# Optimization experiments

Measured on AMD Instinct MI355X. Metric: run time of the kernel, lower is better.

The kernel has to match this reference:

```python
import jax, jax.numpy as jnp
import numpy as np

N = 50000      # nodes
E = 800000     # edges (avg degree 16)
D = 128        # in_dim
H = 128        # hidden_dim
C = 10         # num_classes
G = 128        # graphs in batch
NUM_LAYERS = 3


def setup_inputs() -> dict:
    key = jax.random.key(0)
    ks = jax.random.split(key, 32)
    inp = {
        'features': jax.random.normal(ks[0], (N, D), dtype=jnp.float32),
        'src': jax.random.randint(ks[1], (E,), 0, N, dtype=jnp.int32),
        'dst': jax.random.randint(ks[2], (E,), 0, N, dtype=jnp.int32),
        'graph_ids': jnp.sort(jax.random.randint(ks[3], (N,), 0, G, dtype=jnp.int32)),
        'eps': jnp.zeros((NUM_LAYERS,), dtype=jnp.float32),  # learn_eps=True, init 0
    }
    # GIN MLPs: layer i has linear1 [in,H], linear2 [H,H] (stored as [in,out])
    ki = 4
    for i in range(NUM_LAYERS):
        din = D if i == 0 else H
        inp[f'w1_{i}'] = jax.random.normal(ks[ki], (din, H), dtype=jnp.float32) * (1.0 / np.sqrt(din)); ki += 1
        inp[f'b1_{i}'] = jnp.zeros((H,), dtype=jnp.float32)
        inp[f'w2_{i}'] = jax.random.normal(ks[ki], (H, H), dtype=jnp.float32) * (1.0 / np.sqrt(H)); ki += 1
        inp[f'b2_{i}'] = jnp.zeros((H,), dtype=jnp.float32)
    inp['wc1'] = jax.random.normal(ks[ki], (H, H), dtype=jnp.float32) * (1.0 / np.sqrt(H)); ki += 1
    inp['bc1'] = jnp.zeros((H,), dtype=jnp.float32)
    inp['wc2'] = jax.random.normal(ks[ki], (H, C), dtype=jnp.float32) * (1.0 / np.sqrt(H)); ki += 1
    inp['bc2'] = jnp.zeros((C,), dtype=jnp.float32)
    return inp


def _mlp(x, w1, b1, w2, b2):
    return jax.nn.relu(x @ w1 + b1) @ w2 + b2


def reference(features, src, dst, graph_ids, eps,
              w1_0, b1_0, w2_0, b2_0,
              w1_1, b1_1, w2_1, b2_1,
              w1_2, b1_2, w2_2, b2_2,
              wc1, bc1, wc2, bc2):
    mlps = [(w1_0, b1_0, w2_0, b2_0), (w1_1, b1_1, w2_1, b2_1), (w1_2, b1_2, w2_2, b2_2)]
    h = features
    for i, (w1, b1, w2, b2) in enumerate(mlps):
        # GINConv: aggregate sum of in-neighbor features (gather src, segment-sum into dst)
        agg = jax.ops.segment_sum(h[src], dst, num_segments=N)
        h = (1.0 + eps[i]) * h + agg
        h = _mlp(h, w1, b1, w2, b2)
        h = jax.nn.relu(h)
    # SumPooling: nodes -> graphs
    hg = jax.ops.segment_sum(h, graph_ids, num_segments=G)  # [G, H]
    out = jax.nn.relu(hg @ wc1 + bc1) @ wc2 + bc2            # [G, C]
    return out
```

## Files before the change

### kernel.cpp

```cpp
#include <hip/hip_runtime.h>

#define NN 50000
#define EE 800000
#define HH 128
#define CC 10
#define GG 128
#define NBK 782
#define NCH 98
#define CHUNK 8192

typedef __attribute__((ext_vector_type(8))) short short8;
typedef __attribute__((ext_vector_type(4))) float f32x4;

__device__ __forceinline__ ushort f2b(float f) {
    union { float f; uint u; } x; x.f = f;
    uint u = x.u;
    uint r = (u + 0x7fffu + ((u >> 16) & 1u)) >> 16;
    return (ushort)r;
}
__device__ __forceinline__ float lo2f(uint v) {
    union { uint u; float f; } x; x.u = v << 16; return x.f;
}
__device__ __forceinline__ float hi2f(uint v) {
    union { uint u; float f; } x; x.u = v & 0xffff0000u; return x.f;
}


__global__ __launch_bounds__(256) void prep_kernel(const float* __restrict__ features,
                                                   const float* w0, const float* w1,
                                                   const float* w2, const float* w3,
                                                   const float* w4, const float* w5,
                                                   const int* __restrict__ dst,
                                                   ushort* __restrict__ hb0,
                                                   ushort* __restrict__ wt,
                                                   int* __restrict__ hist,
                                                   float* __restrict__ hg) {
    __shared__ int hc[NBK];
    const int b = blockIdx.x, t = threadIdx.x;
    if (b < 6250) {
        int idx = b * 256 + t;
        float4 v = *(const float4*)(features + (size_t)idx * 4);
        ushort4 o;
        o.x = f2b(v.x); o.y = f2b(v.y); o.z = f2b(v.z); o.w = f2b(v.w);
        *(ushort4*)(hb0 + (size_t)idx * 4) = o;
    } else if (b < 6634) {
        int idx = (b - 6250) * 256 + t;
        int mi = idx >> 14, rest = idx & 16383;
        int n = rest >> 7, k = rest & 127;
        const float* src;
        switch (mi) {
            case 0: src = w0; break; case 1: src = w1; break;
            case 2: src = w2; break; case 3: src = w3; break;
            case 4: src = w4; break; default: src = w5; break;
        }
        wt[mi * 16384 + n * 128 + k] = f2b(src[k * 128 + n]);
    } else if (b < 6732) {
        const int c = b - 6634;
        for (int k = t; k < NBK; k += 256) hc[k] = 0;
        __syncthreads();
        for (int j = 0; j < 32; ++j) {
            int e = c * CHUNK + j * 256 + t;
            if (e < EE) atomicAdd(&hc[dst[e] >> 6], 1);
        }
        __syncthreads();
        for (int k = t; k < NBK; k += 256) hist[k * NCH + c] = hc[k];
    } else {
        int idx = (b - 6732) * 256 + t;
        hg[idx] = 0.f;
    }
}

__global__ __launch_bounds__(128) void bscan_kernel(const int* __restrict__ hist,
                                                    int* __restrict__ rel,
                                                    int* __restrict__ btot) {
    __shared__ int s[128];
    const int b = blockIdx.x, t = threadIdx.x;
    int v = (t < NCH) ? hist[b * NCH + t] : 0;
    s[t] = v;
    __syncthreads();
    for (int off = 1; off < 128; off <<= 1) {
        int tt = (t >= off) ? s[t - off] : 0;
        __syncthreads();
        s[t] += tt;
        __syncthreads();
    }
    if (t < NCH) rel[b * NCH + t] = s[t] - v;
    if (t == 127) btot[b] = s[127];
}

__global__ __launch_bounds__(1024) void tscan_kernel(const int* __restrict__ btot,
                                                     int* __restrict__ bucketptr,
                                                     int* __restrict__ rowptr) {
    __shared__ int s[1024];
    const int t = threadIdx.x;
    int v = (t < NBK) ? btot[t] : 0;
    s[t] = v;
    __syncthreads();
    for (int off = 1; off < 1024; off <<= 1) {
        int tt = (t >= off) ? s[t - off] : 0;
        __syncthreads();
        s[t] += tt;
        __syncthreads();
    }
    if (t < NBK) bucketptr[t] = s[t] - v;
    if (t == 0) { bucketptr[NBK] = EE; rowptr[NN] = EE; }
}

__global__ __launch_bounds__(256) void scatter_kernel(const int* __restrict__ src,
                                                      const int* __restrict__ dst,
                                                      const int* __restrict__ rel,
                                                      const int* __restrict__ bucketptr,
                                                      int* __restrict__ epk) {
    __shared__ int cur[NBK];
    const int c = blockIdx.x, t = threadIdx.x;
    for (int k = t; k < NBK; k += 256) cur[k] = bucketptr[k] + rel[k * NCH + c];
    __syncthreads();
    for (int j = 0; j < 32; ++j) {
        int e = c * CHUNK + j * 256 + t;
        if (e < EE) {
            int d = dst[e];
            int bk = d >> 6;
            int pos = atomicAdd(&cur[bk], 1);
            epk[pos] = ((d & 63) << 16) | src[e];
        }
    }
}

__global__ __launch_bounds__(256) void bsort_kernel(const int* __restrict__ epk,
                                                    const int* __restrict__ bucketptr,
                                                    ushort* __restrict__ eidx,
                                                    int* __restrict__ rowptr) {
    __shared__ int cnt[64];
    __shared__ int cur[64];
    const int b = blockIdx.x, t = threadIdx.x;
    const int base = bucketptr[b], end = bucketptr[b + 1];
    if (t < 64) cnt[t] = 0;
    __syncthreads();
    for (int i = base + t; i < end; i += 256)
        atomicAdd(&cnt[(epk[i] >> 16) & 63], 1);
    __syncthreads();
    if (t < 64) {
        int v = cnt[t];
        int incl = v;
#pragma unroll
        for (int off = 1; off < 64; off <<= 1) {
            int u = __shfl_up(incl, off);
            if (t >= off) incl += u;
        }
        int excl = incl - v;
        cur[t] = excl;
        int node = b * 64 + t;
        if (node < NN) rowptr[node] = base + excl;
    }
    __syncthreads();
    for (int i = base + t; i < end; i += 256) {
        int p = epk[i];
        int dl = (p >> 16) & 63;
        int pos = atomicAdd(&cur[dl], 1);
        eidx[base + pos] = (ushort)(p & 0xffff);
    }
}


__global__ __launch_bounds__(256) void aggregate_kernel(const ushort* __restrict__ h,
                                                        const int* __restrict__ rowptr,
                                                        const ushort* __restrict__ eidx,
                                                        const float* __restrict__ epsp,
                                                        int layer,
                                                        ushort* __restrict__ xb) {
    const int node = blockIdx.x * 8 + (threadIdx.x >> 5);
    if (node >= NN) return;
    const int li = threadIdx.x & 31;
    const int beg = rowptr[node], end = rowptr[node + 1];
    float c0 = 0.f, c1 = 0.f, c2 = 0.f, c3 = 0.f;
    int i = beg;
    for (; i + 8 <= end; i += 8) {
        int s[8];
        uint2 v[8];
#pragma unroll
        for (int k = 0; k < 8; ++k) s[k] = eidx[i + k];
#pragma unroll
        for (int k = 0; k < 8; ++k)
            v[k] = *(const uint2*)(h + (size_t)s[k] * HH + li * 4);
#pragma unroll
        for (int k = 0; k < 8; ++k) {
            c0 += lo2f(v[k].x); c1 += hi2f(v[k].x);
            c2 += lo2f(v[k].y); c3 += hi2f(v[k].y);
        }
    }
    if (i < end) {
        int s[8];
        uint2 v[8];
#pragma unroll
        for (int k = 0; k < 8; ++k) {
            int idx = i + k;
            s[k] = eidx[idx < end ? idx : end - 1];
        }
#pragma unroll
        for (int k = 0; k < 8; ++k)
            v[k] = *(const uint2*)(h + (size_t)s[k] * HH + li * 4);
#pragma unroll
        for (int k = 0; k < 8; ++k) {
            if (i + k < end) {
                c0 += lo2f(v[k].x); c1 += hi2f(v[k].x);
                c2 += lo2f(v[k].y); c3 += hi2f(v[k].y);
            }
        }
    }
    uint2 hv = *(const uint2*)(h + (size_t)node * HH + li * 4);
    const float e = 1.0f + epsp[layer];
    ushort4 o;
    o.x = f2b(e * lo2f(hv.x) + c0);
    o.y = f2b(e * hi2f(hv.x) + c1);
    o.z = f2b(e * lo2f(hv.y) + c2);
    o.w = f2b(e * hi2f(hv.y) + c3);
    *(ushort4*)(xb + (size_t)node * HH + li * 4) = o;
}


template <bool LAST>
__global__ __launch_bounds__(256) void fused_mlp(const ushort* __restrict__ xb,
                                                 const ushort* __restrict__ wt1,
                                                 const ushort* __restrict__ wt2,
                                                 const float* __restrict__ b1,
                                                 const float* __restrict__ b2,
                                                 const int* __restrict__ gid,
                                                 float* __restrict__ hg,
                                                 ushort* __restrict__ out, int nrows) {
    __shared__ __align__(16) ushort xs[2][64][136];
    __shared__ __align__(16) ushort hs[64][136];
    const int tid = threadIdx.x;
    const int lane = tid & 63, w = tid >> 6;
    const int row0 = blockIdx.x * 128;
    const int l15 = lane & 15, lhi = lane >> 4;
    const int sr = tid >> 4, skq = tid & 15;

    uint4 st[4];
#pragma unroll
    for (int it = 0; it < 4; ++it) {
        int r = it * 16 + sr;
        int row = row0 + r;
        st[it] = make_uint4(0u, 0u, 0u, 0u);
        if (row < nrows) st[it] = *(const uint4*)(xb + (size_t)row * HH + skq * 8);
    }

    short8 a1[2][4], a2[2][4];
#pragma unroll
    for (int fa = 0; fa < 2; ++fa)
#pragma unroll
        for (int kt = 0; kt < 4; ++kt) {
            int n = w * 32 + fa * 16 + l15;
            int k = kt * 32 + lhi * 8;
            a1[fa][kt] = *(const short8*)(wt1 + n * HH + k);
            a2[fa][kt] = *(const short8*)(wt2 + n * HH + k);
        }

#pragma unroll
    for (int it = 0; it < 4; ++it) *(uint4*)&xs[0][it * 16 + sr][skq * 8] = st[it];
    __syncthreads();

#pragma unroll
    for (int it = 0; it < 4; ++it) {
        int r = it * 16 + sr;
        int row = row0 + 64 + r;
        st[it] = make_uint4(0u, 0u, 0u, 0u);
        if (row < nrows) st[it] = *(const uint4*)(xb + (size_t)row * HH + skq * 8);
    }

    f32x4 acc[2][4];
#pragma unroll
    for (int tile = 0; tile < 2; ++tile) {
        const int rt0 = row0 + tile * 64;
#pragma unroll
        for (int fa = 0; fa < 2; ++fa)
#pragma unroll
            for (int fb = 0; fb < 4; ++fb) acc[fa][fb] = (f32x4)(0.f);
#pragma unroll
        for (int kt = 0; kt < 4; ++kt) {
            short8 bfr[4];
#pragma unroll
            for (int fb = 0; fb < 4; ++fb)
                bfr[fb] = *(const short8*)&xs[tile][fb * 16 + l15][kt * 32 + lhi * 8];
#pragma unroll
            for (int fa = 0; fa < 2; ++fa)
#pragma unroll
                for (int fb = 0; fb < 4; ++fb)
                    acc[fa][fb] = __builtin_amdgcn_mfma_f32_16x16x32_bf16(a1[fa][kt], bfr[fb],
                                                                         acc[fa][fb], 0, 0, 0);
        }
#pragma unroll
        for (int fa = 0; fa < 2; ++fa) {
            int nb = w * 32 + fa * 16 + lhi * 4;
            float4 bv = *(const float4*)(b1 + nb);
#pragma unroll
            for (int fb = 0; fb < 4; ++fb) {
                ushort4 o;
                o.x = f2b(fmaxf(acc[fa][fb][0] + bv.x, 0.f));
                o.y = f2b(fmaxf(acc[fa][fb][1] + bv.y, 0.f));
                o.z = f2b(fmaxf(acc[fa][fb][2] + bv.z, 0.f));
                o.w = f2b(fmaxf(acc[fa][fb][3] + bv.w, 0.f));
                *(ushort4*)&hs[fb * 16 + l15][nb] = o;
            }
        }
        __syncthreads();
#pragma unroll
        for (int fa = 0; fa < 2; ++fa)
#pragma unroll
            for (int fb = 0; fb < 4; ++fb) acc[fa][fb] = (f32x4)(0.f);
#pragma unroll
        for (int kt = 0; kt < 4; ++kt) {
            short8 bfr[4];
#pragma unroll
            for (int fb = 0; fb < 4; ++fb)
                bfr[fb] = *(const short8*)&hs[fb * 16 + l15][kt * 32 + lhi * 8];
#pragma unroll
            for (int fa = 0; fa < 2; ++fa)
#pragma unroll
                for (int fb = 0; fb < 4; ++fb)
                    acc[fa][fb] = __builtin_amdgcn_mfma_f32_16x16x32_bf16(a2[fa][kt], bfr[fb],
                                                                         acc[fa][fb], 0, 0, 0);
        }
#pragma unroll
        for (int fa = 0; fa < 2; ++fa) {
            int nb = w * 32 + fa * 16 + lhi * 4;
            float4 bv = *(const float4*)(b2 + nb);
#pragma unroll
            for (int fb = 0; fb < 4; ++fb) {
                int m = rt0 + fb * 16 + l15;
                ushort4 o;
                o.x = f2b(fmaxf(acc[fa][fb][0] + bv.x, 0.f));
                o.y = f2b(fmaxf(acc[fa][fb][1] + bv.y, 0.f));
                o.z = f2b(fmaxf(acc[fa][fb][2] + bv.z, 0.f));
                o.w = f2b(fmaxf(acc[fa][fb][3] + bv.w, 0.f));
                if (LAST) {
                    *(ushort4*)&xs[tile][fb * 16 + l15][nb] = o;
                } else if (m < nrows) {
                    *(ushort4*)(out + (size_t)m * HH + nb) = o;
                }
            }
        }
        if (tile == 0) {
#pragma unroll
            for (int it = 0; it < 4; ++it) *(uint4*)&xs[1][it * 16 + sr][skq * 8] = st[it];
        }
        __syncthreads();
        if (LAST) {
            int j = tid & 63;
            int rg = tid >> 6;
            float ax = 0.f, ay = 0.f;
            int gcur = -1;
#pragma unroll
            for (int ii = 0; ii < 16; ++ii) {
                int r = rg + ii * 4;
                int n = rt0 + r;
                if (n >= nrows) break;
                int g = gid[n];
                if (g != gcur) {
                    if (gcur >= 0) {
                        atomicAdd(&hg[gcur * HH + 2 * j], ax);
                        atomicAdd(&hg[gcur * HH + 2 * j + 1], ay);
                    }
                    gcur = g; ax = 0.f; ay = 0.f;
                }
                uint v = *(const uint*)&xs[tile][r][2 * j];
                ax += lo2f(v); ay += hi2f(v);
            }
            if (gcur >= 0) {
                atomicAdd(&hg[gcur * HH + 2 * j], ax);
                atomicAdd(&hg[gcur * HH + 2 * j + 1], ay);
            }
        }
    }
}


__global__ __launch_bounds__(128) void classify_kernel(const float* __restrict__ hg,
                                                       const float* __restrict__ wc1,
                                                       const float* __restrict__ bc1,
                                                       const float* __restrict__ wc2,
                                                       const float* __restrict__ bc2,
                                                       float* __restrict__ out) {
    __shared__ float xrow[HH];
    __shared__ float trow[HH];
    int g = blockIdx.x, j = threadIdx.x;
    xrow[j] = hg[g * HH + j];
    __syncthreads();
    float s = bc1[j];
#pragma unroll 8
    for (int k = 0; k < HH; ++k) s += xrow[k] * wc1[k * HH + j];
    trow[j] = fmaxf(s, 0.f);
    __syncthreads();
    if (j < CC) {
        float o = bc2[j];
#pragma unroll 8
        for (int k = 0; k < HH; ++k) o += trow[k] * wc2[k * CC + j];
        out[g * CC + j] = o;
    }
}

extern "C" void kernel_launch(void* const* d_in, const int* in_sizes, int n_in,
                              void* d_out, int out_size, void* d_ws, size_t ws_size,
                              hipStream_t stream) {
    const float* features = (const float*)d_in[0];
    const int* src = (const int*)d_in[1];
    const int* dst = (const int*)d_in[2];
    const int* gid = (const int*)d_in[3];
    const float* eps = (const float*)d_in[4];
    const float* w1[3] = {(const float*)d_in[5], (const float*)d_in[9], (const float*)d_in[13]};
    const float* b1[3] = {(const float*)d_in[6], (const float*)d_in[10], (const float*)d_in[14]};
    const float* w2[3] = {(const float*)d_in[7], (const float*)d_in[11], (const float*)d_in[15]};
    const float* b2[3] = {(const float*)d_in[8], (const float*)d_in[12], (const float*)d_in[16]};
    const float* wc1 = (const float*)d_in[17];
    const float* bc1 = (const float*)d_in[18];
    const float* wc2 = (const float*)d_in[19];
    const float* bc2 = (const float*)d_in[20];
    float* outp = (float*)d_out;

    char* ws = (char*)d_ws;
    size_t off = 0;
    auto alloc = [&](size_t bytes) {
        void* p = ws + off;
        off += (bytes + 255) & ~(size_t)255;
        return p;
    };
    int* hist = (int*)alloc((size_t)NBK * NCH * sizeof(int));
    int* rel = (int*)alloc((size_t)NBK * NCH * sizeof(int));
    int* btot = (int*)alloc(NBK * sizeof(int));
    int* bucketptr = (int*)alloc((NBK + 1) * sizeof(int));
    int* epk = (int*)alloc(EE * sizeof(int));
    ushort* eidx = (ushort*)alloc(EE * sizeof(ushort));
    int* rowptr = (int*)alloc((NN + 1) * sizeof(int));
    ushort* hb0 = (ushort*)alloc((size_t)NN * HH * 2);
    ushort* hbuf = (ushort*)alloc((size_t)NN * HH * 2);
    ushort* xb = (ushort*)alloc((size_t)NN * HH * 2);
    ushort* wtb = (ushort*)alloc(6 * 16384 * 2);
    float* hg = (float*)alloc(GG * HH * sizeof(float));

    prep_kernel<<<6796, 256, 0, stream>>>(features, w1[0], w2[0], w1[1], w2[1], w1[2], w2[2],
                                          dst, hb0, wtb, hist, hg);
    bscan_kernel<<<NBK, 128, 0, stream>>>(hist, rel, btot);
    tscan_kernel<<<1, 1024, 0, stream>>>(btot, bucketptr, rowptr);
    scatter_kernel<<<NCH, 256, 0, stream>>>(src, dst, rel, bucketptr, epk);
    bsort_kernel<<<NBK, 256, 0, stream>>>(epk, bucketptr, eidx, rowptr);

    const int GB = (NN + 127) / 128;
    const int AB = (NN + 7) / 8;

    aggregate_kernel<<<AB, 256, 0, stream>>>(hb0, rowptr, eidx, eps, 0, xb);
    fused_mlp<false><<<GB, 256, 0, stream>>>(xb, wtb + 0 * 16384, wtb + 1 * 16384,
                                             b1[0], b2[0], gid, hg, hbuf, NN);
    aggregate_kernel<<<AB, 256, 0, stream>>>(hbuf, rowptr, eidx, eps, 1, xb);
    fused_mlp<false><<<GB, 256, 0, stream>>>(xb, wtb + 2 * 16384, wtb + 3 * 16384,
                                             b1[1], b2[1], gid, hg, hbuf, NN);
    aggregate_kernel<<<AB, 256, 0, stream>>>(hbuf, rowptr, eidx, eps, 2, xb);
    fused_mlp<true><<<GB, 256, 0, stream>>>(xb, wtb + 4 * 16384, wtb + 5 * 16384,
                                            b1[2], b2[2], gid, hg, nullptr, NN);

    classify_kernel<<<GG, 128, 0, stream>>>(hg, wc1, bc1, wc2, bc2, outp);
}
```

Baseline: 206.9 us.

## Replace bucket scan kernel with atomic base allocation and widen fused MLP blocks

The single-block scan over bucket totals is removed. Each bucket now claims its output base with an atomicAdd on a global counter, so buckets are laid out in arbitrary order, and explicit per-node begin and end arrays replace the contiguous rowptr. Separately, the fused MLP kernel runs 512 threads per block: two 64-row groups are processed concurrently by separate warp sets, instead of one group of 4 waves looping over two tiles with software prefetch. This saves a kernel launch and a serial scan, and raises parallelism in the MLP, at the cost of losing the prefetch overlap and doubling LDS use per block.

```diff
diff --git a/kernel.cpp b/kernel.cpp
--- a/kernel.cpp
+++ b/kernel.cpp
@@ -34,7 +34,8 @@
                                                    ushort* __restrict__ hb0,
                                                    ushort* __restrict__ wt,
                                                    int* __restrict__ hist,
-                                                   float* __restrict__ hg) {
+                                                   float* __restrict__ hg,
+                                                   int* __restrict__ counter) {
     __shared__ int hc[NBK];
     const int b = blockIdx.x, t = threadIdx.x;
     if (b < 6250) {
@@ -67,12 +68,15 @@
     } else {
         int idx = (b - 6732) * 256 + t;
         hg[idx] = 0.f;
+        if (b == 6732 && t == 0) *counter = 0;
     }
 }
 
 __global__ __launch_bounds__(128) void bscan_kernel(const int* __restrict__ hist,
                                                     int* __restrict__ rel,
-                                                    int* __restrict__ btot) {
+                                                    int* __restrict__ btot,
+                                                    int* __restrict__ bucketbase,
+                                                    int* __restrict__ counter) {
     __shared__ int s[128];
     const int b = blockIdx.x, t = threadIdx.x;
     int v = (t < NCH) ? hist[b * NCH + t] : 0;
@@ -85,35 +89,20 @@
         __syncthreads();
     }
     if (t < NCH) rel[b * NCH + t] = s[t] - v;
-    if (t == 127) btot[b] = s[127];
-}
-
-__global__ __launch_bounds__(1024) void tscan_kernel(const int* __restrict__ btot,
-                                                     int* __restrict__ bucketptr,
-                                                     int* __restrict__ rowptr) {
-    __shared__ int s[1024];
-    const int t = threadIdx.x;
-    int v = (t < NBK) ? btot[t] : 0;
-    s[t] = v;
-    __syncthreads();
-    for (int off = 1; off < 1024; off <<= 1) {
-        int tt = (t >= off) ? s[t - off] : 0;
-        __syncthreads();
-        s[t] += tt;
-        __syncthreads();
-    }
-    if (t < NBK) bucketptr[t] = s[t] - v;
-    if (t == 0) { bucketptr[NBK] = EE; rowptr[NN] = EE; }
+    if (t == 127) {
+        btot[b] = s[127];
+        bucketbase[b] = atomicAdd(counter, s[127]);
+    }
 }
 
 __global__ __launch_bounds__(256) void scatter_kernel(const int* __restrict__ src,
                                                       const int* __restrict__ dst,
                                                       const int* __restrict__ rel,
-                                                      const int* __restrict__ bucketptr,
+                                                      const int* __restrict__ bucketbase,
                                                       int* __restrict__ epk) {
     __shared__ int cur[NBK];
     const int c = blockIdx.x, t = threadIdx.x;
-    for (int k = t; k < NBK; k += 256) cur[k] = bucketptr[k] + rel[k * NCH + c];
+    for (int k = t; k < NBK; k += 256) cur[k] = bucketbase[k] + rel[k * NCH + c];
     __syncthreads();
     for (int j = 0; j < 32; ++j) {
         int e = c * CHUNK + j * 256 + t;
@@ -127,13 +116,15 @@
 }
 
 __global__ __launch_bounds__(256) void bsort_kernel(const int* __restrict__ epk,
-                                                    const int* __restrict__ bucketptr,
+                                                    const int* __restrict__ bucketbase,
+                                                    const int* __restrict__ btot,
                                                     ushort* __restrict__ eidx,
-                                                    int* __restrict__ rowptr) {
+                                                    int* __restrict__ rowbeg,
+                                                    int* __restrict__ rowend) {
     __shared__ int cnt[64];
     __shared__ int cur[64];
     const int b = blockIdx.x, t = threadIdx.x;
-    const int base = bucketptr[b], end = bucketptr[b + 1];
+    const int base = bucketbase[b], end = base + btot[b];
     if (t < 64) cnt[t] = 0;
     __syncthreads();
     for (int i = base + t; i < end; i += 256)
@@ -150,7 +141,10 @@
         int excl = incl - v;
         cur[t] = excl;
         int node = b * 64 + t;
-        if (node < NN) rowptr[node] = base + excl;
+        if (node < NN) {
+            rowbeg[node] = base + excl;
+            rowend[node] = base + incl;
+        }
     }
     __syncthreads();
     for (int i = base + t; i < end; i += 256) {
@@ -163,7 +157,8 @@
 
 
 __global__ __launch_bounds__(256) void aggregate_kernel(const ushort* __restrict__ h,
-                                                        const int* __restrict__ rowptr,
+                                                        const int* __restrict__ rowbeg,
+                                                        const int* __restrict__ rowend,
                                                         const ushort* __restrict__ eidx,
                                                         const float* __restrict__ epsp,
                                                         int layer,
@@ -171,7 +166,7 @@
     const int node = blockIdx.x * 8 + (threadIdx.x >> 5);
     if (node >= NN) return;
     const int li = threadIdx.x & 31;
-    const int beg = rowptr[node], end = rowptr[node + 1];
+    const int beg = rowbeg[node], end = rowend[node];
     float c0 = 0.f, c1 = 0.f, c2 = 0.f, c3 = 0.f;
     int i = beg;
     for (; i + 8 <= end; i += 8) {
@@ -219,7 +214,7 @@
 
 
 template <bool LAST>
-__global__ __launch_bounds__(256) void fused_mlp(const ushort* __restrict__ xb,
+__global__ __launch_bounds__(512) void fused_mlp(const ushort* __restrict__ xb,
                                                  const ushort* __restrict__ wt1,
                                                  const ushort* __restrict__ wt2,
                                                  const float* __restrict__ b1,
@@ -228,20 +223,23 @@
                                                  float* __restrict__ hg,
                                                  ushort* __restrict__ out, int nrows) {
     __shared__ __align__(16) ushort xs[2][64][136];
-    __shared__ __align__(16) ushort hs[64][136];
+    __shared__ __align__(16) ushort hs[2][64][136];
     const int tid = threadIdx.x;
-    const int lane = tid & 63, w = tid >> 6;
-    const int row0 = blockIdx.x * 128;
+    const int lane = tid & 63;
+    const int w = (tid >> 6) & 3;
+    const int g = tid >> 8;
+    const int row0 = blockIdx.x * 128 + g * 64;
     const int l15 = lane & 15, lhi = lane >> 4;
-    const int sr = tid >> 4, skq = tid & 15;
-
-    uint4 st[4];
+    const int gt = tid & 255;
+    const int sr = gt >> 4, skq = gt & 15;
+
 #pragma unroll
     for (int it = 0; it < 4; ++it) {
         int r = it * 16 + sr;
         int row = row0 + r;
-        st[it] = make_uint4(0u, 0u, 0u, 0u);
-        if (row < nrows) st[it] = *(const uint4*)(xb + (size_t)row * HH + skq * 8);
+        uint4 xv = make_uint4(0u, 0u, 0u, 0u);
+        if (row < nrows) xv = *(const uint4*)(xb + (size_t)row * HH + skq * 8);
+        *(uint4*)&xs[g][r][skq * 8] = xv;
     }
 
     short8 a1[2][4], a2[2][4];
@@ -254,121 +252,106 @@
             a1[fa][kt] = *(const short8*)(wt1 + n * HH + k);
             a2[fa][kt] = *(const short8*)(wt2 + n * HH + k);
         }
-
-#pragma unroll
-    for (int it = 0; it < 4; ++it) *(uint4*)&xs[0][it * 16 + sr][skq * 8] = st[it];
-    __syncthreads();
-
-#pragma unroll
-    for (int it = 0; it < 4; ++it) {
-        int r = it * 16 + sr;
-        int row = row0 + 64 + r;
-        st[it] = make_uint4(0u, 0u, 0u, 0u);
-        if (row < nrows) st[it] = *(const uint4*)(xb + (size_t)row * HH + skq * 8);
-    }
+    __syncthreads();
 
     f32x4 acc[2][4];
 #pragma unroll
-    for (int tile = 0; tile < 2; ++tile) {
-        const int rt0 = row0 + tile * 64;
+    for (int fa = 0; fa < 2; ++fa)
+#pragma unroll
+        for (int fb = 0; fb < 4; ++fb) acc[fa][fb] = (f32x4)(0.f);
+#pragma unroll
+    for (int kt = 0; kt < 4; ++kt) {
+        short8 bfr[4];
+#pragma unroll
+        for (int fb = 0; fb < 4; ++fb)
+            bfr[fb] = *(const short8*)&xs[g][fb * 16 + l15][kt * 32 + lhi * 8];
 #pragma unroll
         for (int fa = 0; fa < 2; ++fa)
 #pragma unroll
-            for (int fb = 0; fb < 4; ++fb) acc[fa][fb] = (f32x4)(0.f);
-#pragma unroll
-        for (int kt = 0; kt < 4; ++kt) {
-            short8 bfr[4];
-#pragma unroll
             for (int fb = 0; fb < 4; ++fb)
-                bfr[fb] = *(const short8*)&xs[tile][fb * 16 + l15][kt * 32 + lhi * 8];
-#pragma unroll
-            for (int fa = 0; fa < 2; ++fa)
-#pragma unroll
-                for (int fb = 0; fb < 4; ++fb)
-                    acc[fa][fb] = __builtin_amdgcn_mfma_f32_16x16x32_bf16(a1[fa][kt], bfr[fb],
-                                                                         acc[fa][fb], 0, 0, 0);
-        }
-#pragma unroll
-        for (int fa = 0; fa < 2; ++fa) {
-            int nb = w * 32 + fa * 16 + lhi * 4;
-            float4 bv = *(const float4*)(b1 + nb);
-#pragma unroll
-            for (int fb = 0; fb < 4; ++fb) {
-                ushort4 o;
-                o.x = f2b(fmaxf(acc[fa][fb][0] + bv.x, 0.f));
-                o.y = f2b(fmaxf(acc[fa][fb][1] + bv.y, 0.f));
-                o.z = f2b(fmaxf(acc[fa][fb][2] + bv.z, 0.f));
-                o.w = f2b(fmaxf(acc[fa][fb][3] + bv.w, 0.f));
-                *(ushort4*)&hs[fb * 16 + l15][nb] = o;
+                acc[fa][fb] = __builtin_amdgcn_mfma_f32_16x16x32_bf16(a1[fa][kt], bfr[fb],
+                                                                     acc[fa][fb], 0, 0, 0);
+    }
+
+#pragma unroll
+    for (int fa = 0; fa < 2; ++fa) {
+        int nb = w * 32 + fa * 16 + lhi * 4;
+        float4 bv = *(const float4*)(b1 + nb);
+#pragma unroll
+        for (int fb = 0; fb < 4; ++fb) {
+            ushort4 o;
+            o.x = f2b(fmaxf(acc[fa][fb][0] + bv.x, 0.f));
+            o.y = f2b(fmaxf(acc[fa][fb][1] + bv.y, 0.f));
+            o.z = f2b(fmaxf(acc[fa][fb][2] + bv.z, 0.f));
+            o.w = f2b(fmaxf(acc[fa][fb][3] + bv.w, 0.f));
+            *(ushort4*)&hs[g][fb * 16 + l15][nb] = o;
+        }
+    }
+    __syncthreads();
+
+#pragma unroll
+    for (int fa = 0; fa < 2; ++fa)
+#pragma unroll
+        for (int fb = 0; fb < 4; ++fb) acc[fa][fb] = (f32x4)(0.f);
+#pragma unroll
+    for (int kt = 0; kt < 4; ++kt) {
+        short8 bfr[4];
+#pragma unroll
+        for (int fb = 0; fb < 4; ++fb)
+            bfr[fb] = *(const short8*)&hs[g][fb * 16 + l15][kt * 32 + lhi * 8];
+#pragma unroll
+        for (int fa = 0; fa < 2; ++fa)
+#pragma unroll
+            for (int fb = 0; fb < 4; ++fb)
+                acc[fa][fb] = __builtin_amdgcn_mfma_f32_16x16x32_bf16(a2[fa][kt], bfr[fb],
+                                                                     acc[fa][fb], 0, 0, 0);
+    }
+
+#pragma unroll
+    for (int fa = 0; fa < 2; ++fa) {
+        int nb = w * 32 + fa * 16 + lhi * 4;
+        float4 bv = *(const float4*)(b2 + nb);
+#pragma unroll
+        for (int fb = 0; fb < 4; ++fb) {
+            int m = row0 + fb * 16 + l15;
+            ushort4 o;
+            o.x = f2b(fmaxf(acc[fa][fb][0] + bv.x, 0.f));
+            o.y = f2b(fmaxf(acc[fa][fb][1] + bv.y, 0.f));
+            o.z = f2b(fmaxf(acc[fa][fb][2] + bv.z, 0.f));
+            o.w = f2b(fmaxf(acc[fa][fb][3] + bv.w, 0.f));
+            if (LAST) {
+                *(ushort4*)&xs[g][fb * 16 + l15][nb] = o;
+            } else if (m < nrows) {
+                *(ushort4*)(out + (size_t)m * HH + nb) = o;
             }
         }
+    }
+
+    if (LAST) {
         __syncthreads();
-#pragma unroll
-        for (int fa = 0; fa < 2; ++fa)
-#pragma unroll
-            for (int fb = 0; fb < 4; ++fb) acc[fa][fb] = (f32x4)(0.f);
-#pragma unroll
-        for (int kt = 0; kt < 4; ++kt) {
-            short8 bfr[4];
-#pragma unroll
-            for (int fb = 0; fb < 4; ++fb)
-                bfr[fb] = *(const short8*)&hs[fb * 16 + l15][kt * 32 + lhi * 8];
-#pragma unroll
-            for (int fa = 0; fa < 2; ++fa)
-#pragma unroll
-                for (int fb = 0; fb < 4; ++fb)
-                    acc[fa][fb] = __builtin_amdgcn_mfma_f32_16x16x32_bf16(a2[fa][kt], bfr[fb],
-                                                                         acc[fa][fb], 0, 0, 0);
-        }
-#pragma unroll
-        for (int fa = 0; fa < 2; ++fa) {
-            int nb = w * 32 + fa * 16 + lhi * 4;
-            float4 bv = *(const float4*)(b2 + nb);
-#pragma unroll
-            for (int fb = 0; fb < 4; ++fb) {
-                int m = rt0 + fb * 16 + l15;
-                ushort4 o;
-                o.x = f2b(fmaxf(acc[fa][fb][0] + bv.x, 0.f));
-                o.y = f2b(fmaxf(acc[fa][fb][1] + bv.y, 0.f));
-                o.z = f2b(fmaxf(acc[fa][fb][2] + bv.z, 0.f));
-                o.w = f2b(fmaxf(acc[fa][fb][3] + bv.w, 0.f));
-                if (LAST) {
-                    *(ushort4*)&xs[tile][fb * 16 + l15][nb] = o;
-                } else if (m < nrows) {
-                    *(ushort4*)(out + (size_t)m * HH + nb) = o;
+        int j = gt & 63;
+        int rg = gt >> 6;
+        float ax = 0.f, ay = 0.f;
+        int gcur = -1;
+#pragma unroll
+        for (int ii = 0; ii < 16; ++ii) {
+            int r = rg + ii * 4;
+            int n = row0 + r;
+            if (n >= nrows) break;
+            int gv = gid[n];
+            if (gv != gcur) {
+                if (gcur >= 0) {
+                    atomicAdd(&hg[gcur * HH + 2 * j], ax);
+                    atomicAdd(&hg[gcur * HH + 2 * j + 1], ay);
                 }
+                gcur = gv; ax = 0.f; ay = 0.f;
             }
-        }
-        if (tile == 0) {
-#pragma unroll
-            for (int it = 0; it < 4; ++it) *(uint4*)&xs[1][it * 16 + sr][skq * 8] = st[it];
-        }
-        __syncthreads();
-        if (LAST) {
-            int j = tid & 63;
-            int rg = tid >> 6;
-            float ax = 0.f, ay = 0.f;
-            int gcur = -1;
-#pragma unroll
-            for (int ii = 0; ii < 16; ++ii) {
-                int r = rg + ii * 4;
-                int n = rt0 + r;
-                if (n >= nrows) break;
-                int g = gid[n];
-                if (g != gcur) {
-                    if (gcur >= 0) {
-                        atomicAdd(&hg[gcur * HH + 2 * j], ax);
-                        atomicAdd(&hg[gcur * HH + 2 * j + 1], ay);
-                    }
-                    gcur = g; ax = 0.f; ay = 0.f;
-                }
-                uint v = *(const uint*)&xs[tile][r][2 * j];
-                ax += lo2f(v); ay += hi2f(v);
-            }
-            if (gcur >= 0) {
-                atomicAdd(&hg[gcur * HH + 2 * j], ax);
-                atomicAdd(&hg[gcur * HH + 2 * j + 1], ay);
-            }
+            uint v = *(const uint*)&xs[g][r][2 * j];
+            ax += lo2f(v); ay += hi2f(v);
+        }
+        if (gcur >= 0) {
+            atomicAdd(&hg[gcur * HH + 2 * j], ax);
+            atomicAdd(&hg[gcur * HH + 2 * j + 1], ay);
         }
     }
 }
@@ -426,10 +409,12 @@
     int* hist = (int*)alloc((size_t)NBK * NCH * sizeof(int));
     int* rel = (int*)alloc((size_t)NBK * NCH * sizeof(int));
     int* btot = (int*)alloc(NBK * sizeof(int));
-    int* bucketptr = (int*)alloc((NBK + 1) * sizeof(int));
+    int* bucketbase = (int*)alloc(NBK * sizeof(int));
+    int* counter = (int*)alloc(256);
     int* epk = (int*)alloc(EE * sizeof(int));
     ushort* eidx = (ushort*)alloc(EE * sizeof(ushort));
-    int* rowptr = (int*)alloc((NN + 1) * sizeof(int));
+    int* rowbeg = (int*)alloc(NN * sizeof(int));
+    int* rowend = (int*)alloc(NN * sizeof(int));
     ushort* hb0 = (ushort*)alloc((size_t)NN * HH * 2);
     ushort* hbuf = (ushort*)alloc((size_t)NN * HH * 2);
     ushort* xb = (ushort*)alloc((size_t)NN * HH * 2);
@@ -437,23 +422,22 @@
     float* hg = (float*)alloc(GG * HH * sizeof(float));
 
     prep_kernel<<<6796, 256, 0, stream>>>(features, w1[0], w2[0], w1[1], w2[1], w1[2], w2[2],
-                                          dst, hb0, wtb, hist, hg);
-    bscan_kernel<<<NBK, 128, 0, stream>>>(hist, rel, btot);
-    tscan_kernel<<<1, 1024, 0, stream>>>(btot, bucketptr, rowptr);
-    scatter_kernel<<<NCH, 256, 0, stream>>>(src, dst, rel, bucketptr, epk);
-    bsort_kernel<<<NBK, 256, 0, stream>>>(epk, bucketptr, eidx, rowptr);
+                                          dst, hb0, wtb, hist, hg, counter);
+    bscan_kernel<<<NBK, 128, 0, stream>>>(hist, rel, btot, bucketbase, counter);
+    scatter_kernel<<<NCH, 256, 0, stream>>>(src, dst, rel, bucketbase, epk);
+    bsort_kernel<<<NBK, 256, 0, stream>>>(epk, bucketbase, btot, eidx, rowbeg, rowend);
 
     const int GB = (NN + 127) / 128;
     const int AB = (NN + 7) / 8;
 
-    aggregate_kernel<<<AB, 256, 0, stream>>>(hb0, rowptr, eidx, eps, 0, xb);
-    fused_mlp<false><<<GB, 256, 0, stream>>>(xb, wtb + 0 * 16384, wtb + 1 * 16384,
+    aggregate_kernel<<<AB, 256, 0, stream>>>(hb0, rowbeg, rowend, eidx, eps, 0, xb);
+    fused_mlp<false><<<GB, 512, 0, stream>>>(xb, wtb + 0 * 16384, wtb + 1 * 16384,
                                              b1[0], b2[0], gid, hg, hbuf, NN);
-    aggregate_kernel<<<AB, 256, 0, stream>>>(hbuf, rowptr, eidx, eps, 1, xb);
-    fused_mlp<false><<<GB, 256, 0, stream>>>(xb, wtb + 2 * 16384, wtb + 3 * 16384,
+    aggregate_kernel<<<AB, 256, 0, stream>>>(hbuf, rowbeg, rowend, eidx, eps, 1, xb);
+    fused_mlp<false><<<GB, 512, 0, stream>>>(xb, wtb + 2 * 16384, wtb + 3 * 16384,
                                              b1[1], b2[1], gid, hg, hbuf, NN);
-    aggregate_kernel<<<AB, 256, 0, stream>>>(hbuf, rowptr, eidx, eps, 2, xb);
-    fused_mlp<true><<<GB, 256, 0, stream>>>(xb, wtb + 4 * 16384, wtb + 5 * 16384,
+    aggregate_kernel<<<AB, 256, 0, stream>>>(hbuf, rowbeg, rowend, eidx, eps, 2, xb);
+    fused_mlp<true><<<GB, 512, 0, stream>>>(xb, wtb + 4 * 16384, wtb + 5 * 16384,
                                             b1[2], b2[2], gid, hg, nullptr, NN);
 
     classify_kernel<<<GG, 128, 0, stream>>>(hg, wc1, bc1, wc2, bc2, outp);
```

Measured after the change: 213.9 us. 3.4% more time.
